# Kernel optimization log

Hardware: AMD Instinct MI355X
Metric: run time of the kernel (lower is better)

Reference implementation:

```python
import jax, jax.numpy as jnp
import numpy as np

ATT = 32      # att_size per spatial dim (pooled grid is 32x32, N=1024)
HEADS = 8

def _pool_sum(x, out):
    # adaptive max + adaptive avg pool (exact uniform windows since W%out==0)
    B, C, W, H = x.shape
    kw, kh = W // out, H // out
    r = x.reshape(B, C, out, kw, out, kh)
    return r.max(axis=(3, 5)) + r.mean(axis=(3, 5))

def _lerp_axis(x, out_len, axis):
    in_len = x.shape[axis]
    pos = jnp.arange(out_len, dtype=x.dtype) * ((in_len - 1) / (out_len - 1))
    i0 = jnp.floor(pos).astype(jnp.int32)
    i1 = jnp.minimum(i0 + 1, in_len - 1)
    t = pos - i0.astype(x.dtype)
    shp = [1] * x.ndim
    shp[axis] = out_len
    t = t.reshape(shp)
    return jnp.take(x, i0, axis=axis) * (1 - t) + jnp.take(x, i1, axis=axis) * t

def _upsample_bilinear_ac(x, out_h, out_w):
    # bilinear, align_corners=True (separable)
    return _lerp_axis(_lerp_axis(x, out_h, 2), out_w, 3)

def setup_inputs() -> dict:
    key = jax.random.key(0)
    k1, k2, k3, k4 = jax.random.split(key, 4)
    B, C, W, H = 8, 256, 128, 128
    input1 = jax.random.normal(k1, (B, C, W, H), dtype=jnp.float32)
    input2 = jax.random.normal(k2, (B, C // 2, W, H), dtype=jnp.float32)
    # 1x1 conv: out=C, in=C//2 (kaiming-ish scale)
    conv_w = jax.random.normal(k3, (C, C // 2), dtype=jnp.float32) * (1.0 / np.sqrt(C // 2))
    conv_b = jax.random.normal(k4, (C,), dtype=jnp.float32) * 0.01
    return {"input1": input1, "input2": input2, "conv_w": conv_w, "conv_b": conv_b}

def reference(input1, input2, conv_w, conv_b):
    B, C, W, H = input1.shape
    # channel projection (1x1 conv) since input2 has C//2 channels
    x2 = jnp.einsum('bihw,oi->bohw', input2, conv_w) + conv_b[None, :, None, None]
    p1 = _pool_sum(input1, ATT)   # [B,C,32,32]
    p2 = _pool_sum(x2, ATT)
    N = ATT * ATT
    q = p1.reshape(B, C, N).transpose(2, 0, 1)  # [N,B,C]
    k = p2.reshape(B, C, N).transpose(2, 0, 1)
    v = k
    scale = 1.0 / np.sqrt(C // HEADS)
    w = jnp.einsum('nbc,nec->nbe', q, k)        # [N,B,B]
    w = jax.nn.softmax(w * scale, axis=-1)
    a = jnp.einsum('nbe,nec->nbc', w, v)        # [N,B,C]
    attn = a.transpose(1, 2, 0).reshape(B, C, ATT, ATT)
    up = _upsample_bilinear_ac(attn, W, H)
    return jax.nn.sigmoid(up)
```

## Files before the change

kernel.cpp:

```cpp
#include <hip/hip_runtime.h>
#include <math.h>

namespace {

constexpr int Bn = 8, Cn = 256, CIN = 128, Wd = 128, Hd = 128, ATTn = 32, Nn = ATTn * ATTn;

typedef __attribute__((ext_vector_type(8))) short short8;
typedef __attribute__((ext_vector_type(4))) float f32x4;

__device__ inline unsigned short bf16_rne(float f) {
    unsigned int u = __float_as_uint(f);
    unsigned int r = (u + 0x7FFFu + ((u >> 16) & 1u)) >> 16;
    return (unsigned short)r;
}

__global__ __launch_bounds__(256) void pool1_kernel(const float* __restrict__ in,
                                                    float* __restrict__ p1) {
    int idx = blockIdx.x * 256 + threadIdx.x;
    int ox = idx & 31;
    int oy = (idx >> 5) & 31;
    int bc = idx >> 10;
    const float* base = in + ((size_t)bc * Wd + oy * 4) * Hd + ox * 4;
    float mx = -INFINITY, sm = 0.f;
#pragma unroll
    for (int dy = 0; dy < 4; ++dy) {
        float4 v = *reinterpret_cast<const float4*>(base + dy * Hd);
        mx = fmaxf(mx, fmaxf(fmaxf(v.x, v.y), fmaxf(v.z, v.w)));
        sm += (v.x + v.y) + (v.z + v.w);
    }
    p1[idx] = mx + sm * (1.f / 16.f);
}

__global__ __launch_bounds__(512) void convpool_kernel(const float* __restrict__ in2,
                                                       const float* __restrict__ cw,
                                                       const float* __restrict__ cb,
                                                       float* __restrict__ p2t) {
    __shared__ __align__(16) unsigned char sIn[2][16384];

    const int t = threadIdx.x;
    const int w = t >> 6;
    const int l = t & 63;
    const int bid = blockIdx.x;
    const int b = bid >> 6;
    const int oy = (bid >> 1) & 31;
    const int half = bid & 1;

    const int n_lo = l & 15;
    const int khi = l >> 4;

    short8 bfrag[2][4];
#pragma unroll
    for (int f = 0; f < 2; ++f) {
        const int n = w * 32 + f * 16 + n_lo;
#pragma unroll
        for (int kk = 0; kk < 4; ++kk) {
            const float* wp = cw + n * CIN + kk * 32 + khi * 8;
            float4 va = *reinterpret_cast<const float4*>(wp);
            float4 vb = *reinterpret_cast<const float4*>(wp + 4);
            short8 s;
            s[0] = (short)bf16_rne(va.x); s[1] = (short)bf16_rne(va.y);
            s[2] = (short)bf16_rne(va.z); s[3] = (short)bf16_rne(va.w);
            s[4] = (short)bf16_rne(vb.x); s[5] = (short)bf16_rne(vb.y);
            s[6] = (short)bf16_rne(vb.z); s[7] = (short)bf16_rne(vb.w);
            bfrag[f][kk] = s;
        }
    }
    const float bias2_0 = 2.f * cb[w * 32 + n_lo];
    const float bias2_1 = 2.f * cb[w * 32 + 16 + n_lo];

    const int xq = t & 3, dy = (t >> 2) & 3, k4 = t >> 4;
    const int row = oy * 4 + dy;
    const float* src = in2 + (((size_t)(b * CIN + k4 * 4)) * Wd + row) * Hd + half * 64 + xq * 4;

    float4 r0, r1, r2, r3;
#define STAGE_LOAD(g)                                                   \
    {   const float* p_ = src + (g) * 16;                               \
        r0 = *reinterpret_cast<const float4*>(p_);                      \
        r1 = *reinterpret_cast<const float4*>(p_ + Wd * Hd);            \
        r2 = *reinterpret_cast<const float4*>(p_ + 2 * Wd * Hd);        \
        r3 = *reinterpret_cast<const float4*>(p_ + 3 * Wd * Hd); }

#define WRQ(buf, dx, c0, c1, c2, c3)                                    \
    {   const int px_ = dy * 4 + (dx);                                  \
        uint2 u_;                                                       \
        u_.x = (unsigned int)bf16_rne(c0) | ((unsigned int)bf16_rne(c1) << 16); \
        u_.y = (unsigned int)bf16_rne(c2) | ((unsigned int)bf16_rne(c3) << 16); \
        const int off_ = (xq * 4096 + px_ * 256 + k4 * 8) ^ (((px_ & 7) << 4) ^ ((xq & 3) << 5)); \
        *reinterpret_cast<uint2*>(&sIn[buf][off_]) = u_; }

#define STAGE_WRITE(buf)                                                \
    {   WRQ(buf, 0, r0.x, r1.x, r2.x, r3.x)                             \
        WRQ(buf, 1, r0.y, r1.y, r2.y, r3.y)                             \
        WRQ(buf, 2, r0.z, r1.z, r2.z, r3.z)                             \
        WRQ(buf, 3, r0.w, r1.w, r2.w, r3.w) }

    STAGE_LOAD(0)
    STAGE_WRITE(0)
    __syncthreads();

    const int px = n_lo;
    for (int g = 0; g < 4; ++g) {
        const int buf = g & 1;
        if (g < 3) STAGE_LOAD(g + 1)

        const unsigned char* base = sIn[buf];
#pragma unroll
        for (int c = 0; c < 4; ++c) {
            const int swz = ((px & 7) << 4) ^ ((c & 3) << 5);
            f32x4 acc0 = {0.f, 0.f, 0.f, 0.f};
            f32x4 acc1 = {0.f, 0.f, 0.f, 0.f};
#pragma unroll
            for (int kk = 0; kk < 4; ++kk) {
                short8 a = *reinterpret_cast<const short8*>(
                    base + ((c * 4096 + px * 256 + kk * 64 + khi * 16) ^ swz));
                acc0 = __builtin_amdgcn_mfma_f32_16x16x32_bf16(a, bfrag[0][kk], acc0, 0, 0, 0);
                acc1 = __builtin_amdgcn_mfma_f32_16x16x32_bf16(a, bfrag[1][kk], acc1, 0, 0, 0);
            }
            float mx0 = fmaxf(fmaxf(acc0[0], acc0[1]), fmaxf(acc0[2], acc0[3]));
            float sm0 = (acc0[0] + acc0[1]) + (acc0[2] + acc0[3]);
            float mx1 = fmaxf(fmaxf(acc1[0], acc1[1]), fmaxf(acc1[2], acc1[3]));
            float sm1 = (acc1[0] + acc1[1]) + (acc1[2] + acc1[3]);
            mx0 = fmaxf(mx0, __shfl_xor(mx0, 16)); sm0 += __shfl_xor(sm0, 16);
            mx0 = fmaxf(mx0, __shfl_xor(mx0, 32)); sm0 += __shfl_xor(sm0, 32);
            mx1 = fmaxf(mx1, __shfl_xor(mx1, 16)); sm1 += __shfl_xor(sm1, 16);
            mx1 = fmaxf(mx1, __shfl_xor(mx1, 32)); sm1 += __shfl_xor(sm1, 32);
            if (l < 16) {
                const int cell = oy * 32 + half * 16 + g * 4 + c;
                float* dst = p2t + ((size_t)b * Nn + cell) * Cn + w * 32 + n_lo;
                dst[0]  = mx0 + sm0 * (1.f / 16.f) + bias2_0;
                dst[16] = mx1 + sm1 * (1.f / 16.f) + bias2_1;
            }
        }

        if (g < 3) STAGE_WRITE((g + 1) & 1)
        __syncthreads();
    }
#undef STAGE_LOAD
#undef STAGE_WRITE
#undef WRQ
}

__global__ __launch_bounds__(256) void attn_kernel(const float* __restrict__ p1,
                                                   const float* __restrict__ p2t,
                                                   float* __restrict__ att) {
    __shared__ float q[Bn][Cn + 1];
    __shared__ float kk[Bn][Cn + 1];
    __shared__ float wsm[Bn][8];
    int n = blockIdx.x, t = threadIdx.x;

#pragma unroll
    for (int i = 0; i < 8; ++i) {
        int flat = t + i * 256;
        int bb = flat >> 8, c = flat & 255;
        q[bb][c]  = p1[((size_t)bb * Cn + c) * Nn + n];
        kk[bb][c] = p2t[((size_t)bb * Nn + n) * Cn + c];
    }
    __syncthreads();

    if (t < 64) {
        int bb = t >> 3, e = t & 7;
        float s = 0.f;
        for (int c = 0; c < Cn; ++c) s = fmaf(q[bb][c], kk[e][c], s);
        wsm[bb][e] = s * 0.17677669529663687f;
    }
    __syncthreads();

    if (t < 8) {
        float mx = -INFINITY;
#pragma unroll
        for (int e = 0; e < 8; ++e) mx = fmaxf(mx, wsm[t][e]);
        float sum = 0.f;
#pragma unroll
        for (int e = 0; e < 8; ++e) {
            float v = __expf(wsm[t][e] - mx);
            wsm[t][e] = v;
            sum += v;
        }
        float inv = 1.f / sum;
#pragma unroll
        for (int e = 0; e < 8; ++e) wsm[t][e] *= inv;
    }
    __syncthreads();

    float kv[8];
#pragma unroll
    for (int e = 0; e < 8; ++e) kv[e] = kk[e][t];
#pragma unroll
    for (int bb = 0; bb < 8; ++bb) {
        float s = 0.f;
#pragma unroll
        for (int e = 0; e < 8; ++e) s = fmaf(wsm[bb][e], kv[e], s);
        att[((size_t)bb * Cn + t) * Nn + n] = s;
    }
}

__global__ __launch_bounds__(256) void upsample_kernel(const float* __restrict__ att,
                                                       float* __restrict__ out) {
    __shared__ float tile[ATTn * ATTn];
    int bc = blockIdx.x, t = threadIdx.x;
    reinterpret_cast<float4*>(tile)[t] =
        reinterpret_cast<const float4*>(att + (size_t)bc * Nn)[t];
    __syncthreads();

    int tx = t & 31, ty = t >> 5;
    int xi0[4], xi1[4];
    float xt[4];
#pragma unroll
    for (int j = 0; j < 4; ++j) {
        int x = tx * 4 + j;
        float pos = (float)x * (31.f / 127.f);
        int i0 = (int)pos;
        xi0[j] = i0;
        xi1[j] = min(i0 + 1, 31);
        xt[j] = pos - (float)i0;
    }

    for (int r = 0; r < 16; ++r) {
        int y = ty + r * 8;
        float posy = (float)y * (31.f / 127.f);
        int y0 = (int)posy;
        int y1 = min(y0 + 1, 31);
        float ft = posy - (float)y0;
        float o_[4];
#pragma unroll
        for (int j = 0; j < 4; ++j) {
            float v00 = tile[y0 * 32 + xi0[j]];
            float v01 = tile[y0 * 32 + xi1[j]];
            float v10 = tile[y1 * 32 + xi0[j]];
            float v11 = tile[y1 * 32 + xi1[j]];
            float top = v00 * (1.f - ft) + v10 * ft;
            float bot = v01 * (1.f - ft) + v11 * ft;
            float val = top * (1.f - xt[j]) + bot * xt[j];
            o_[j] = 1.f / (1.f + __expf(-val));
        }
        *reinterpret_cast<float4*>(out + ((size_t)bc * Wd + y) * Hd + tx * 4) =
            make_float4(o_[0], o_[1], o_[2], o_[3]);
    }
}

}

extern "C" void kernel_launch(void* const* d_in, const int* in_sizes, int n_in,
                              void* d_out, int out_size, void* d_ws, size_t ws_size,
                              hipStream_t stream) {
    const float* input1 = (const float*)d_in[0];
    const float* input2 = (const float*)d_in[1];
    const float* conv_w = (const float*)d_in[2];
    const float* conv_b = (const float*)d_in[3];
    float* out = (float*)d_out;

    float* p1  = (float*)d_ws;
    float* p2t = p1 + (size_t)Bn * Cn * Nn;
    float* att = p2t + (size_t)Bn * Cn * Nn;

    pool1_kernel<<<dim3(Bn * Cn * Nn / 256), dim3(256), 0, stream>>>(input1, p1);
    convpool_kernel<<<dim3(512), dim3(512), 0, stream>>>(input2, conv_w, conv_b, p2t);
    attn_kernel<<<dim3(Nn), dim3(256), 0, stream>>>(p1, p2t, att);
    upsample_kernel<<<dim3(Bn * Cn), dim3(256), 0, stream>>>(att, out);
}
```

Measured before the change: 124.3 us.

## Fuse input1 pooling into conv-pool kernel with transposed output and parallel softmax

Merges the input1 max+avg pooling into the conv-pool launch by giving it extra blocks, so both pooling stages share one launch and can overlap. Pooled input1 is now written in [B,N,C] layout, which lets the attention kernel load q and k with coalesced float4 reads instead of strided gathers. The attention kernel also spreads the 8x8 dot products over all 256 threads and does the softmax with wavefront shuffles, replacing the 64-thread and 8-thread serial phases. The cost is that pooling writes are now strided across channels, and pool blocks hold 32 registers each.

```diff
diff --git a/kernel.cpp b/kernel.cpp
--- a/kernel.cpp
+++ b/kernel.cpp
@@ -14,33 +14,44 @@
     return (unsigned short)r;
 }
 
-__global__ __launch_bounds__(256) void pool1_kernel(const float* __restrict__ in,
-                                                    float* __restrict__ p1) {
-    int idx = blockIdx.x * 256 + threadIdx.x;
-    int ox = idx & 31;
-    int oy = (idx >> 5) & 31;
-    int bc = idx >> 10;
-    const float* base = in + ((size_t)bc * Wd + oy * 4) * Hd + ox * 4;
-    float mx = -INFINITY, sm = 0.f;
-#pragma unroll
-    for (int dy = 0; dy < 4; ++dy) {
-        float4 v = *reinterpret_cast<const float4*>(base + dy * Hd);
-        mx = fmaxf(mx, fmaxf(fmaxf(v.x, v.y), fmaxf(v.z, v.w)));
-        sm += (v.x + v.y) + (v.z + v.w);
-    }
-    p1[idx] = mx + sm * (1.f / 16.f);
-}
-
-__global__ __launch_bounds__(512) void convpool_kernel(const float* __restrict__ in2,
-                                                       const float* __restrict__ cw,
-                                                       const float* __restrict__ cb,
-                                                       float* __restrict__ p2t) {
+__global__ __launch_bounds__(512) void front_kernel(const float* __restrict__ in1,
+                                                    const float* __restrict__ in2,
+                                                    const float* __restrict__ cw,
+                                                    const float* __restrict__ cb,
+                                                    float* __restrict__ p1t,
+                                                    float* __restrict__ p2t) {
     __shared__ __align__(16) unsigned char sIn[2][16384];
 
     const int t = threadIdx.x;
+    const int bid = blockIdx.x;
+
+    if (bid >= 512) {
+        const int bid2 = bid - 512;
+        const int b = bid2 >> 5, oy = bid2 & 31;
+        const int c = t & 255, xh = t >> 8;
+        const float* src = in1 + (((size_t)(b * Cn + c) * Wd + oy * 4)) * Hd + xh * 64;
+        float mx[16], sm[16];
+#pragma unroll
+        for (int q = 0; q < 16; ++q) { mx[q] = -INFINITY; sm[q] = 0.f; }
+#pragma unroll
+        for (int dy = 0; dy < 4; ++dy) {
+            const float4* rp = reinterpret_cast<const float4*>(src + dy * Hd);
+#pragma unroll
+            for (int q = 0; q < 16; ++q) {
+                float4 v = rp[q];
+                mx[q] = fmaxf(mx[q], fmaxf(fmaxf(v.x, v.y), fmaxf(v.z, v.w)));
+                sm[q] += (v.x + v.y) + (v.z + v.w);
+            }
+        }
+        float* dst = p1t + ((size_t)b * Nn + oy * 32 + xh * 16) * Cn + c;
+#pragma unroll
+        for (int q = 0; q < 16; ++q)
+            dst[(size_t)q * Cn] = mx[q] + sm[q] * (1.f / 16.f);
+        return;
+    }
+
     const int w = t >> 6;
     const int l = t & 63;
-    const int bid = blockIdx.x;
     const int b = bid >> 6;
     const int oy = (bid >> 1) & 31;
     const int half = bid & 1;
@@ -140,45 +151,42 @@
 #undef WRQ
 }
 
-__global__ __launch_bounds__(256) void attn_kernel(const float* __restrict__ p1,
+__global__ __launch_bounds__(256) void attn_kernel(const float* __restrict__ p1t,
                                                    const float* __restrict__ p2t,
                                                    float* __restrict__ att) {
-    __shared__ float q[Bn][Cn + 1];
-    __shared__ float kk[Bn][Cn + 1];
+    __shared__ float q[Bn][260];
+    __shared__ float kk[Bn][260];
     __shared__ float wsm[Bn][8];
-    int n = blockIdx.x, t = threadIdx.x;
-
-#pragma unroll
-    for (int i = 0; i < 8; ++i) {
-        int flat = t + i * 256;
-        int bb = flat >> 8, c = flat & 255;
-        q[bb][c]  = p1[((size_t)bb * Cn + c) * Nn + n];
-        kk[bb][c] = p2t[((size_t)bb * Nn + n) * Cn + c];
-    }
-    __syncthreads();
-
-    if (t < 64) {
-        int bb = t >> 3, e = t & 7;
+    const int n = blockIdx.x, t = threadIdx.x;
+
+#pragma unroll
+    for (int i = 0; i < 2; ++i) {
+        const int f = t + i * 256;
+        const int bb = f >> 6, cq = f & 63;
+        const size_t off = ((size_t)bb * Nn + n) * Cn + cq * 4;
+        *reinterpret_cast<float4*>(&q[bb][cq * 4])  = *reinterpret_cast<const float4*>(p1t + off);
+        *reinterpret_cast<float4*>(&kk[bb][cq * 4]) = *reinterpret_cast<const float4*>(p2t + off);
+    }
+    __syncthreads();
+
+    {
+        const int chunk = t & 3, pair = t >> 2;
+        const int e = pair & 7, bb = pair >> 3;
         float s = 0.f;
-        for (int c = 0; c < Cn; ++c) s = fmaf(q[bb][c], kk[e][c], s);
-        wsm[bb][e] = s * 0.17677669529663687f;
-    }
-    __syncthreads();
-
-    if (t < 8) {
-        float mx = -INFINITY;
-#pragma unroll
-        for (int e = 0; e < 8; ++e) mx = fmaxf(mx, wsm[t][e]);
-        float sum = 0.f;
-#pragma unroll
-        for (int e = 0; e < 8; ++e) {
-            float v = __expf(wsm[t][e] - mx);
-            wsm[t][e] = v;
-            sum += v;
-        }
-        float inv = 1.f / sum;
-#pragma unroll
-        for (int e = 0; e < 8; ++e) wsm[t][e] *= inv;
+#pragma unroll
+        for (int i = 0; i < 64; ++i)
+            s = fmaf(q[bb][i * 4 + chunk], kk[e][i * 4 + chunk], s);
+        s += __shfl_xor(s, 1);
+        s += __shfl_xor(s, 2);
+        s *= 0.17677669529663687f;
+        float m = fmaxf(s, __shfl_xor(s, 4));
+        m = fmaxf(m, __shfl_xor(m, 8));
+        m = fmaxf(m, __shfl_xor(m, 16));
+        float p = __expf(s - m);
+        float d = p + __shfl_xor(p, 4);
+        d += __shfl_xor(d, 8);
+        d += __shfl_xor(d, 16);
+        if (chunk == 0) wsm[bb][e] = p / d;
     }
     __syncthreads();
 
@@ -249,12 +257,11 @@
     const float* conv_b = (const float*)d_in[3];
     float* out = (float*)d_out;
 
-    float* p1  = (float*)d_ws;
-    float* p2t = p1 + (size_t)Bn * Cn * Nn;
+    float* p1t = (float*)d_ws;
+    float* p2t = p1t + (size_t)Bn * Cn * Nn;
     float* att = p2t + (size_t)Bn * Cn * Nn;
 
-    pool1_kernel<<<dim3(Bn * Cn * Nn / 256), dim3(256), 0, stream>>>(input1, p1);
-    convpool_kernel<<<dim3(512), dim3(512), 0, stream>>>(input2, conv_w, conv_b, p2t);
-    attn_kernel<<<dim3(Nn), dim3(256), 0, stream>>>(p1, p2t, att);
+    front_kernel<<<dim3(768), dim3(512), 0, stream>>>(input1, input2, conv_w, conv_b, p1t, p2t);
+    attn_kernel<<<dim3(Nn), dim3(256), 0, stream>>>(p1t, p2t, att);
     upsample_kernel<<<dim3(Bn * Cn), dim3(256), 0, stream>>>(att, out);
 }
```

New measurement: 120.6 us. 1.03x faster.
